# Kernel tuning notes

Measured on AMD Instinct MI355X. Metric: run time of the kernel, lower is better.

The kernel has to match this reference:

```python
import jax, jax.numpy as jnp
import numpy as np

DIM = 1024; H = 16; KVH = 4; HD = 64          # head_dim = DIM // H
I = 2048                                       # intermediate_size = 2*DIM
N = 16                                         # ssm_state_size
DTR = 64                                       # dt_rank = DIM // 16
K = 4                                          # conv kernel
BASE = 10000.0
EPS = 1.1920929e-07                            # torch F.rms_norm default eps (fp32 finfo eps)

def rms_norm(x):
    return x * jax.lax.rsqrt(jnp.mean(x * x, axis=-1, keepdims=True) + EPS)

def rope_tables(S, dims):
    inv = 1.0 / BASE ** (jnp.arange(0, dims, 2, dtype=jnp.float32) / dims)
    f = jnp.outer(jnp.arange(S, dtype=jnp.float32), inv)   # [S, dims//2]
    return jnp.cos(f), jnp.sin(f)

def apply_rope(x, cos, sin):
    half = x.shape[-1] // 2
    x1, x2 = x[..., :half], x[..., half:]
    return jnp.concatenate([x1 * cos + x2 * sin, -x1 * sin + x2 * cos], axis=-1)

def setup_inputs() -> dict:
    key = jax.random.key(0)
    ks = jax.random.split(key, 12)
    B, S = 2, 2048
    def w(k, shape, s=0.02):
        return jax.random.normal(k, shape, jnp.float32) * s
    return {
        "x": jax.random.normal(ks[0], (B, S, DIM), jnp.float32),
        "W_mamba": w(ks[1], (2 * I, DIM)),
        "W_q": w(ks[2], (DIM, DIM)),
        "W_kv": w(ks[3], (2 * KVH * HD, DIM)),
        "q_gain": jnp.full((H,), 1.0, jnp.float32),
        "conv_w": w(ks[4], (I, K), 0.2),
        "conv_b": jnp.zeros((I,), jnp.float32),
        "W_xproj": w(ks[5], (DTR + 2 * N, I)),
        "W_dt": w(ks[6], (I, DTR)),
        "b_dt": w(ks[7], (I,), 0.5),
        "A_log": jnp.log(jnp.broadcast_to(jnp.arange(1, N + 1, dtype=jnp.float32), (I, N))),
        "D": jnp.ones((I,), jnp.float32),
        "W_mamba_out": w(ks[8], (DIM, I)),
        "W_proj": w(ks[9], (DIM, DIM)),
        "merge_alpha": jnp.zeros((1,), jnp.float32),
    }

def reference(x, W_mamba, W_q, W_kv, q_gain, conv_w, conv_b, W_xproj, W_dt, b_dt,
              A_log, D, W_mamba_out, W_proj, merge_alpha):
    B, S, _ = x.shape
    # --- parallel input projection for the mamba branch ---
    mp = x @ W_mamba.T                         # [B,S,2I]
    x_ssm, gate = mp[..., :I], mp[..., I:]
    # --- attention branch (GQA + full RoPE + per-head q gain) ---
    q = (x @ W_q.T).reshape(B, S, H, HD).transpose(0, 2, 1, 3)
    kv = x @ W_kv.T
    k = kv[..., :KVH * HD].reshape(B, S, KVH, HD).transpose(0, 2, 1, 3)
    v = kv[..., KVH * HD:].reshape(B, S, KVH, HD).transpose(0, 2, 1, 3)
    q = rms_norm(q); k = rms_norm(k)
    cos, sin = rope_tables(S, HD)
    q = apply_rope(q, cos, sin)
    k = apply_rope(k, cos, sin)
    q = q * q_gain[None, :, None, None]
    nrep = H // KVH
    k = jnp.repeat(k, nrep, axis=1)
    v = jnp.repeat(v, nrep, axis=1)
    scores = jnp.einsum('bhqd,bhkd->bhqk', q, k) / jnp.sqrt(jnp.float32(HD))
    mask = jnp.tril(jnp.ones((S, S), bool))
    scores = jnp.where(mask, scores, -jnp.inf)
    y = jnp.einsum('bhqk,bhkd->bhqd', jax.nn.softmax(scores, axis=-1), v)
    attn_out = y.transpose(0, 2, 1, 3).reshape(B, S, DIM)
    # --- mamba/SSM branch: causal depthwise conv1d + silu ---
    xc = x_ssm.transpose(0, 2, 1)              # [B,I,S]
    u = jax.lax.conv_general_dilated(xc, conv_w[:, None, :], (1,), [(K - 1, 0)],
                                     dimension_numbers=('NCH', 'OIH', 'NCH'),
                                     feature_group_count=I) + conv_b[None, :, None]
    u = u * jax.nn.sigmoid(u)                  # silu, [B,I,S]
    u_bsi = u.transpose(0, 2, 1)               # [B,S,I]
    params = u_bsi @ W_xproj.T                 # [B,S,DTR+2N]
    dt_low = params[..., :DTR]
    Bm = params[..., DTR:DTR + N]
    Cm = params[..., DTR + N:]
    delta = jax.nn.softplus(dt_low @ W_dt.T + b_dt)   # [B,S,I] (delta_bias + softplus)
    A = -jnp.exp(A_log)                        # [I,N]
    def step(state, inp):
        d_t, b_t, c_t, u_t = inp               # [B,I],[B,N],[B,N],[B,I]
        dA = jnp.exp(d_t[:, :, None] * A[None])
        state = state * dA + d_t[:, :, None] * b_t[:, None, :] * u_t[:, :, None]
        y_t = jnp.sum(state * c_t[:, None, :], axis=-1)
        return state, y_t
    xs = (delta.transpose(1, 0, 2), Bm.transpose(1, 0, 2),
          Cm.transpose(1, 0, 2), u_bsi.transpose(1, 0, 2))
    state0 = jnp.zeros((B, I, N), x.dtype)
    _, ys = jax.lax.scan(step, state0, xs)     # ys: [S,B,I]
    y_ssm = ys.transpose(1, 0, 2) + u_bsi * D  # + D skip
    y_ssm = y_ssm * (gate * jax.nn.sigmoid(gate))      # gated by silu(z)
    mamba_out = y_ssm @ W_mamba_out.T          # [B,S,DIM]
    # --- gated merge + output projection ---
    alpha = jax.nn.sigmoid(merge_alpha)
    merged = alpha * attn_out + (1.0 - alpha) * mamba_out
    return merged @ W_proj.T
```

## Files before the change

kernel.cpp:

```cpp
#include <hip/hip_runtime.h>
#include <hip/hip_bf16.h>

#define B_   2
#define S_   2048
#define T_   4096
#define DIM_ 1024
#define H_   16
#define KVH_ 4
#define HD_  64
#define I_   2048
#define N_   16
#define DTR_ 64
#define MB   ((size_t)1 << 20)

typedef __hip_bfloat16 bf16;
typedef __attribute__((ext_vector_type(8))) short short8;
typedef __attribute__((ext_vector_type(4))) short short4v;
typedef __attribute__((ext_vector_type(4))) float f32x4;

__device__ __forceinline__ float b2f(bf16 v){ return __bfloat162float(v); }
__device__ __forceinline__ bf16  f2b(float v){ return __float2bfloat16(v); }
__device__ __forceinline__ float s2f(short s){
  return __builtin_bit_cast(float, ((unsigned int)(unsigned short)s) << 16);
}
__device__ __forceinline__ short f2s(float v){
  return (short)__builtin_bit_cast(unsigned short, f2b(v));
}

__device__ __forceinline__ void async16(const void* g, void* l) {
  __builtin_amdgcn_global_load_lds((__attribute__((address_space(1))) void*)g,
                                   (__attribute__((address_space(3))) void*)l, 16, 0, 0);
}

__global__ __launch_bounds__(256)
void cast_f2b(const float* __restrict__ in, bf16* __restrict__ out, int n4)
{
  const int i = blockIdx.x * 256 + threadIdx.x;
  if (i >= n4) return;
  const float4 v = ((const float4*)in)[i];
  short4v o;
  o.x = f2s(v.x); o.y = f2s(v.y); o.z = f2s(v.z); o.w = f2s(v.w);
  *(short4v*)(out + (size_t)i * 4) = o;
}

template<int MODE, int TS>
__global__ __launch_bounds__(256)
void gemm_nt(const bf16* __restrict__ A, int lda,
             const bf16* __restrict__ W, int ldw,
             void* __restrict__ C, int ldc,
             bf16* __restrict__ Ct, int ldt,
             const float* __restrict__ bias,
             int M, int N, int K)
{
  __shared__ __align__(16) bf16 As[128*32];
  __shared__ __align__(16) bf16 Bs[128*32];
  const int tid  = threadIdx.x;
  const int lane = tid & 63;
  const int wave = tid >> 6;
  const int l16  = lane & 15;
  const int quad = lane >> 4;
  const int wm   = (wave >> 1) << 6;
  const int wn   = (wave & 1) << 6;
  const int m0   = blockIdx.x << 7;
  const int n0   = blockIdx.y << 7;

  f32x4 acc[4][4];
  const f32x4 zero = {0.f, 0.f, 0.f, 0.f};
  #pragma unroll
  for (int i = 0; i < 4; i++)
    #pragma unroll
    for (int j = 0; j < 4; j++) acc[i][j] = zero;

  for (int k0 = 0; k0 < K; k0 += 32) {
    #pragma unroll
    for (int p = 0; p < 2; p++) {
      const int linear = ((p << 8) + tid) << 4;
      const int row    = linear >> 6;
      const int inrow  = linear & 63;
      async16(A + (size_t)(m0 + row) * lda + k0 + (inrow >> 1), (char*)As + linear);
      int wr = n0 + row; if (wr > N - 1) wr = N - 1;
      async16(W + (size_t)wr * ldw + k0 + (inrow >> 1), (char*)Bs + linear);
    }
    __syncthreads();
    short8 af[4], bfr[4];
    #pragma unroll
    for (int mt = 0; mt < 4; mt++)
      af[mt] = *(const short8*)((const char*)As + ((wm + (mt << 4) + l16) << 6) + (quad << 4));
    #pragma unroll
    for (int nt = 0; nt < 4; nt++)
      bfr[nt] = *(const short8*)((const char*)Bs + ((wn + (nt << 4) + l16) << 6) + (quad << 4));
    #pragma unroll
    for (int mt = 0; mt < 4; mt++)
      #pragma unroll
      for (int nt = 0; nt < 4; nt++)
        acc[mt][nt] = __builtin_amdgcn_mfma_f32_16x16x32_bf16(af[mt], bfr[nt], acc[mt][nt], 0, 0, 0);
    __syncthreads();
  }

  #pragma unroll
  for (int mt = 0; mt < 4; mt++) {
    #pragma unroll
    for (int nt = 0; nt < 4; nt++) {
      const int col = n0 + wn + (nt << 4) + l16;
      if (col >= N) continue;
      const int rowbase = m0 + wm + (mt << 4) + (quad << 2);
      float v[4];
      #pragma unroll
      for (int r = 0; r < 4; r++) {
        float t = acc[mt][nt][r];
        if (MODE == 2) {
          t += bias[col];
          t = (t > 20.f) ? t : log1pf(__expf(t));
        }
        v[r] = t;
      }
      if (TS == 0 || TS == 2) {
        #pragma unroll
        for (int r = 0; r < 4; r++) {
          if (MODE == 0) ((float*)C)[(size_t)(rowbase + r) * ldc + col] = v[r];
          else           ((bf16*)C)[(size_t)(rowbase + r) * ldc + col] = f2b(v[r]);
        }
      }
      if (TS >= 1) {
        short4v p;
        #pragma unroll
        for (int r = 0; r < 4; r++) p[r] = f2s(v[r]);
        *(short4v*)(Ct + (size_t)col * ldt + rowbase) = p;
      }
    }
  }
}

__global__ __launch_bounds__(256)
void qkv_prep(const bf16* __restrict__ qraw, const bf16* __restrict__ kvraw,
              const float* __restrict__ q_gain,
              bf16* __restrict__ qn, bf16* __restrict__ kn, bf16* __restrict__ vt)
{
  const int wid  = blockIdx.x * 4 + (threadIdx.x >> 6);
  const int lane = threadIdx.x & 63;
  const int t    = wid / 24;
  const int slot = wid % 24;
  const int b = t >> 11, s = t & 2047;

  float val;
  if (slot < 16)       val = b2f(qraw [(size_t)t * 1024 + slot * 64 + lane]);
  else if (slot < 20)  val = b2f(kvraw[(size_t)t * 512  + (slot - 16) * 64 + lane]);
  else                 val = b2f(kvraw[(size_t)t * 512  + 256 + (slot - 20) * 64 + lane]);

  if (slot < 20) {
    float ss = val * val;
    #pragma unroll
    for (int off = 32; off; off >>= 1) ss += __shfl_xor(ss, off);
    val *= rsqrtf(ss * (1.0f / 64.0f) + 1.1920929e-07f);
    const int j = lane & 31;
    const float x1 = __shfl(val, j);
    const float x2 = __shfl(val, j + 32);
    const float inv = powf(10000.0f, -(float)j * (1.0f / 32.0f));
    const float ang = (float)s * inv;
    const float c = cosf(ang), sn = sinf(ang);
    val = (lane < 32) ? (x1 * c + x2 * sn) : (x2 * c - x1 * sn);
  }
  if (slot < 16) {
    val *= q_gain[slot];
    qn[((size_t)(b * 16 + slot) * 2048 + s) * 64 + lane] = f2b(val);
  } else if (slot < 20) {
    kn[((size_t)(b * 4 + (slot - 16)) * 2048 + s) * 64 + lane] = f2b(val);
  } else {
    vt[((size_t)(b * 4 + (slot - 20)) * 64 + lane) * 2048 + s] = f2b(val);
  }
}

__global__ __launch_bounds__(256)
void attn_fwd(const bf16* __restrict__ qn, const bf16* __restrict__ kn,
              const bf16* __restrict__ vt, bf16* __restrict__ attn)
{
  __shared__ __align__(16) bf16 Plds[4][16][32];
  const int b = blockIdx.z, h = blockIdx.y, q0 = blockIdx.x * 64;
  const int wave = threadIdx.x >> 6, lane = threadIdx.x & 63;
  const int l16 = lane & 15, quad = lane >> 4;
  const int kvh = h >> 2;
  const bf16* Q  = qn + (size_t)(b * 16 + h)   * 2048 * 64;
  const bf16* Kp = kn + (size_t)(b * 4 + kvh)  * 2048 * 64;
  const bf16* Vt = vt + (size_t)(b * 4 + kvh)  * 64 * 2048;

  const int qrow_l = q0 + wave * 16 + l16;
  const short8 qf0 = *(const short8*)(Q + (size_t)qrow_l * 64 + quad * 8);
  const short8 qf1 = *(const short8*)(Q + (size_t)qrow_l * 64 + 32 + quad * 8);

  f32x4 acc[4];
  const f32x4 zero = {0.f, 0.f, 0.f, 0.f};
  #pragma unroll
  for (int i = 0; i < 4; i++) acc[i] = zero;
  float m_r[4], l_r[4];
  #pragma unroll
  for (int r = 0; r < 4; r++) { m_r[r] = -1e30f; l_r[r] = 0.f; }

  const int nkt = (q0 + 64) >> 5;
  for (int kt = 0; kt < nkt; kt++) {
    const int kb = kt << 5;
    const short8 kfA0 = *(const short8*)(Kp + (size_t)(kb + l16) * 64 + quad * 8);
    const short8 kfA1 = *(const short8*)(Kp + (size_t)(kb + l16) * 64 + 32 + quad * 8);
    const short8 kfB0 = *(const short8*)(Kp + (size_t)(kb + 16 + l16) * 64 + quad * 8);
    const short8 kfB1 = *(const short8*)(Kp + (size_t)(kb + 16 + l16) * 64 + 32 + quad * 8);
    f32x4 sA = zero, sB = zero;
    sA = __builtin_amdgcn_mfma_f32_16x16x32_bf16(qf0, kfA0, sA, 0, 0, 0);
    sA = __builtin_amdgcn_mfma_f32_16x16x32_bf16(qf1, kfA1, sA, 0, 0, 0);
    sB = __builtin_amdgcn_mfma_f32_16x16x32_bf16(qf0, kfB0, sB, 0, 0, 0);
    sB = __builtin_amdgcn_mfma_f32_16x16x32_bf16(qf1, kfB1, sB, 0, 0, 0);

    const int colA = kb + l16, colB = kb + 16 + l16;
    float pA[4], pB[4], alpha[4];
    #pragma unroll
    for (int r = 0; r < 4; r++) {
      const int row = q0 + wave * 16 + quad * 4 + r;
      float a  = sA[r] * 0.125f;
      float bb = sB[r] * 0.125f;
      if (colA > row) a  = -1e30f;
      if (colB > row) bb = -1e30f;
      float tm = fmaxf(a, bb);
      #pragma unroll
      for (int off = 8; off; off >>= 1) tm = fmaxf(tm, __shfl_xor(tm, off));
      const float nm = fmaxf(m_r[r], tm);
      alpha[r] = __expf(m_r[r] - nm);
      m_r[r] = nm;
      const float pa = __expf(a - nm), pb = __expf(bb - nm);
      pA[r] = pa; pB[r] = pb;
      float ps = pa + pb;
      #pragma unroll
      for (int off = 8; off; off >>= 1) ps += __shfl_xor(ps, off);
      l_r[r] = l_r[r] * alpha[r] + ps;
    }
    #pragma unroll
    for (int nt = 0; nt < 4; nt++)
      #pragma unroll
      for (int r = 0; r < 4; r++) acc[nt][r] *= alpha[r];

    __syncthreads();
    #pragma unroll
    for (int r = 0; r < 4; r++) {
      Plds[wave][quad * 4 + r][l16]      = f2b(pA[r]);
      Plds[wave][quad * 4 + r][16 + l16] = f2b(pB[r]);
    }
    __syncthreads();
    const short8 pf = *(const short8*)(&Plds[wave][l16][quad * 8]);
    #pragma unroll
    for (int nt = 0; nt < 4; nt++) {
      const short8 vf = *(const short8*)(Vt + (size_t)(nt * 16 + l16) * 2048 + kb + quad * 8);
      acc[nt] = __builtin_amdgcn_mfma_f32_16x16x32_bf16(pf, vf, acc[nt], 0, 0, 0);
    }
  }

  #pragma unroll
  for (int nt = 0; nt < 4; nt++)
    #pragma unroll
    for (int r = 0; r < 4; r++) {
      const int row = q0 + wave * 16 + quad * 4 + r;
      attn[((size_t)b * 2048 + row) * 1024 + h * 64 + nt * 16 + l16] = f2b(acc[nt][r] / l_r[r]);
    }
}

__global__ __launch_bounds__(256)
void conv_silu_t(const bf16* __restrict__ xssmT, const float* __restrict__ cw,
                 const float* __restrict__ cb,
                 bf16* __restrict__ u, bf16* __restrict__ uT)
{
  const int i = blockIdx.x;
  const int t = blockIdx.y * 256 + threadIdx.x;
  const int s = t & 2047;
  float acc = cb[i];
  #pragma unroll
  for (int kk = 0; kk < 4; kk++) {
    if (s - 3 + kk >= 0)
      acc += s2f(__builtin_bit_cast(short, xssmT[(size_t)i * 4096 + t - 3 + kk])) * cw[i * 4 + kk];
  }
  const float sig = 1.f / (1.f + __expf(-acc));
  const bf16 r = f2b(acc * sig);
  u [(size_t)t * 2048 + i] = r;
  uT[(size_t)i * 4096 + t] = r;
}

__global__ __launch_bounds__(256)
void transpose_bf16(const bf16* __restrict__ in, bf16* __restrict__ out,
                    int R, int C)
{
  __shared__ bf16 tile[64][65];
  const int c0 = blockIdx.x * 64, r0 = blockIdx.y * 64;
  #pragma unroll
  for (int it = 0; it < 2; it++) {
    const int linear = (it * 256 + threadIdx.x) * 8;
    const int r = linear >> 6, cc = linear & 63;
    const short8 v = *(const short8*)(in + (size_t)(r0 + r) * C + c0 + cc);
    #pragma unroll
    for (int k = 0; k < 8; k++)
      tile[r][cc + k] = __builtin_bit_cast(bf16, (unsigned short)v[k]);
  }
  __syncthreads();
  #pragma unroll
  for (int it = 0; it < 2; it++) {
    const int linear = (it * 256 + threadIdx.x) * 8;
    const int oc = linear >> 6, k = linear & 63;
    short8 v;
    #pragma unroll
    for (int kk = 0; kk < 8; kk++)
      v[kk] = (short)__builtin_bit_cast(unsigned short, tile[k + kk][oc]);
    *(short8*)(out + (size_t)(c0 + oc) * R + r0 + k) = v;
  }
}

__global__ __launch_bounds__(256)
void ssm_scan(const bf16* __restrict__ dltT, const bf16* __restrict__ uT,
              const bf16* __restrict__ prmT, const float* __restrict__ A_log,
              const float* __restrict__ Dv, const bf16* __restrict__ gateT,
              bf16* __restrict__ youtT)
{
  __shared__ float Pl[16][17], Fl[16][17], Il[16][17];
  const int blk = blockIdx.x;
  const int b = blk >> 11, i = blk & 2047;
  const int n = threadIdx.x & 15, c = threadIdx.x >> 4;
  const float a  = -__expf(A_log[i * 16 + n]);
  const float Di = Dv[i];
  const size_t rowoff = (size_t)b * 2048 + c * 128;
  const bf16* dp = dltT  + (size_t)i * 4096 + rowoff;
  const bf16* up = uT    + (size_t)i * 4096 + rowoff;
  const bf16* Bp = prmT  + (size_t)(64 + n) * 4096 + rowoff;
  const bf16* Cp = prmT  + (size_t)(80 + n) * 4096 + rowoff;
  const bf16* gp = gateT + (size_t)i * 4096 + rowoff;
  bf16*       yp = youtT + (size_t)i * 4096 + rowoff;

  float P = 1.f, F = 0.f;
  for (int j0 = 0; j0 < 128; j0 += 8) {
    const short8 d8 = *(const short8*)(dp + j0);
    const short8 u8 = *(const short8*)(up + j0);
    const short8 B8 = *(const short8*)(Bp + j0);
    #pragma unroll
    for (int j = 0; j < 8; j++) {
      const float dt = s2f(d8[j]);
      const float dA = __expf(dt * a);
      P *= dA;
      F = F * dA + dt * s2f(u8[j]) * s2f(B8[j]);
    }
  }
  Pl[n][c] = P; Fl[n][c] = F;
  __syncthreads();

  if (threadIdx.x < 16) {
    const int nn = threadIdx.x;
    float s = 0.f;
    #pragma unroll
    for (int cc = 0; cc < 16; cc++) {
      Il[nn][cc] = s;
      s = Fl[nn][cc] + Pl[nn][cc] * s;
    }
  }
  __syncthreads();

  float state = Il[n][c];
  for (int j0 = 0; j0 < 128; j0 += 8) {
    const short8 d8 = *(const short8*)(dp + j0);
    const short8 u8 = *(const short8*)(up + j0);
    const short8 B8 = *(const short8*)(Bp + j0);
    const short8 C8 = *(const short8*)(Cp + j0);
    const short8 g8 = *(const short8*)(gp + j0);
    short8 o8;
    #pragma unroll
    for (int j = 0; j < 8; j++) {
      const float dt = s2f(d8[j]);
      const float ut = s2f(u8[j]);
      const float dA = __expf(dt * a);
      state = state * dA + dt * ut * s2f(B8[j]);
      float y = state * s2f(C8[j]);
      y += __shfl_xor(y, 1); y += __shfl_xor(y, 2);
      y += __shfl_xor(y, 4); y += __shfl_xor(y, 8);
      const float g  = s2f(g8[j]);
      const float gs = g / (1.f + __expf(-g));
      o8[j] = f2s((y + ut * Di) * gs);
    }
    if (n == 0) *(short8*)(yp + j0) = o8;
  }
}

__global__ __launch_bounds__(256)
void merge_k(const bf16* __restrict__ attn, const bf16* __restrict__ mamba,
             const float* __restrict__ malpha, bf16* __restrict__ merged)
{
  const size_t idx = (size_t)blockIdx.x * 256 + threadIdx.x;
  const float al = 1.f / (1.f + __expf(-malpha[0]));
  merged[idx] = f2b(al * b2f(attn[idx]) + (1.f - al) * b2f(mamba[idx]));
}

extern "C" void kernel_launch(void* const* d_in, const int* in_sizes, int n_in,
                              void* d_out, int out_size, void* d_ws, size_t ws_size,
                              hipStream_t stream)
{
  const float* x_f     = (const float*)d_in[0];
  const float* Wm_f    = (const float*)d_in[1];
  const float* Wq_f    = (const float*)d_in[2];
  const float* Wkv_f   = (const float*)d_in[3];
  const float* q_gain  = (const float*)d_in[4];
  const float* conv_w  = (const float*)d_in[5];
  const float* conv_b  = (const float*)d_in[6];
  const float* Wxp_f   = (const float*)d_in[7];
  const float* Wdt_f   = (const float*)d_in[8];
  const float* b_dt    = (const float*)d_in[9];
  const float* A_log   = (const float*)d_in[10];
  const float* Dv      = (const float*)d_in[11];
  const float* Wmo_f   = (const float*)d_in[12];
  const float* Wp_f    = (const float*)d_in[13];
  const float* malpha  = (const float*)d_in[14];

  char* wp = (char*)d_ws;
  bf16*  xb    = (bf16*)(wp + 0 * MB);
  bf16*  Wm_b  = (bf16*)(wp + 8 * MB);
  bf16*  Wq_b  = (bf16*)(wp + 16 * MB);
  bf16*  Wkv_b = (bf16*)(wp + 18 * MB);
  bf16*  xssmT = (bf16*)(wp + 19 * MB);
  bf16*  gateT = (bf16*)(wp + 35 * MB);
  bf16*  u     = (bf16*)(wp + 51 * MB);
  bf16*  uT    = (bf16*)(wp + 67 * MB);
  bf16*  qraw  = (bf16*)(wp + 83 * MB);
  bf16*  kvraw = (bf16*)(wp + 91 * MB);
  bf16*  dltT  = (bf16*)(wp + 95 * MB);
  bf16*  qn    = (bf16*)(wp + 0 * MB);
  bf16*  kn    = (bf16*)(wp + 8 * MB);
  bf16*  vtb   = (bf16*)(wp + 10 * MB);
  bf16*  Wxp_b = (bf16*)(wp + 12 * MB);
  bf16*  Wdt_b = (bf16*)(wp + 12 * MB + 512 * 1024);
  bf16*  prm   = (bf16*)(wp + 13 * MB);
  bf16*  prmT  = (bf16*)(wp + 13 * MB + 768 * 1024);
  bf16*  Wp_b  = (bf16*)(wp + 16 * MB);
  bf16*  attnb = (bf16*)(wp + 83 * MB);
  bf16*  Wmo_b = (bf16*)(wp + 91 * MB);
  bf16*  ybuf  = (bf16*)(wp + 19 * MB);
  bf16*  ybufT = (bf16*)(wp + 51 * MB);
  bf16*  mam   = (bf16*)(wp + 35 * MB);
  bf16*  mrg   = (bf16*)(wp + 43 * MB);
  (void)ws_size; (void)in_sizes; (void)n_in; (void)out_size;

  auto cast = [&](const float* src, bf16* dst, int n) {
    const int n4 = n >> 2;
    cast_f2b<<<dim3((n4 + 255) / 256), 256, 0, stream>>>(src, dst, n4);
  };
  cast(x_f,   xb,    T_ * 1024);
  cast(Wm_f,  Wm_b,  4096 * 1024);
  cast(Wq_f,  Wq_b,  1024 * 1024);
  cast(Wkv_f, Wkv_b, 512 * 1024);

  gemm_nt<1,1><<<dim3(32, 16), 256, 0, stream>>>(xb, 1024, Wm_b,               1024, nullptr, 0, xssmT, 4096, nullptr, T_, 2048, 1024);
  gemm_nt<1,1><<<dim3(32, 16), 256, 0, stream>>>(xb, 1024, Wm_b + 2048 * 1024, 1024, nullptr, 0, gateT, 4096, nullptr, T_, 2048, 1024);
  gemm_nt<1,0><<<dim3(32, 8),  256, 0, stream>>>(xb, 1024, Wq_b,  1024, qraw,  1024, nullptr, 0, nullptr, T_, 1024, 1024);
  gemm_nt<1,0><<<dim3(32, 4),  256, 0, stream>>>(xb, 1024, Wkv_b, 1024, kvraw,  512, nullptr, 0, nullptr, T_,  512, 1024);

  qkv_prep<<<dim3((T_ * 24) / 4), 256, 0, stream>>>(qraw, kvraw, q_gain, qn, kn, vtb);
  conv_silu_t<<<dim3(2048, 16), 256, 0, stream>>>(xssmT, conv_w, conv_b, u, uT);
  attn_fwd<<<dim3(32, 16, 2), 256, 0, stream>>>(qn, kn, vtb, attnb);

  cast(Wxp_f, Wxp_b, 96 * 2048);
  cast(Wdt_f, Wdt_b, 2048 * 64);
  cast(Wmo_f, Wmo_b, 1024 * 2048);
  cast(Wp_f,  Wp_b,  1024 * 1024);

  gemm_nt<1,2><<<dim3(32, 1),  256, 0, stream>>>(u, 2048, Wxp_b, 2048, prm, 96, prmT, 4096, nullptr, T_, 96, 2048);
  gemm_nt<2,1><<<dim3(32, 16), 256, 0, stream>>>(prm, 96, Wdt_b, 64, nullptr, 0, dltT, 4096, b_dt, T_, 2048, 64);
  ssm_scan<<<dim3(4096), 256, 0, stream>>>(dltT, uT, prmT, A_log, Dv, gateT, ybufT);
  transpose_bf16<<<dim3(64, 32), 256, 0, stream>>>(ybufT, ybuf, 2048, 4096);
  gemm_nt<1,0><<<dim3(32, 8),  256, 0, stream>>>(ybuf, 2048, Wmo_b, 2048, mam, 1024, nullptr, 0, nullptr, T_, 1024, 2048);

  merge_k<<<dim3(16384), 256, 0, stream>>>(attnb, mam, malpha, mrg);
  gemm_nt<0,0><<<dim3(32, 8),  256, 0, stream>>>(mrg, 1024, Wp_b, 1024, (float*)d_out, 1024, nullptr, 0, nullptr, T_, 1024, 1024);
}
```

Baseline: 925.6 us.

## Replace strided conv output write with tiled transpose; move gating into transpose kernel

conv_silu_t no longer writes the row-major u buffer with a column-strided, uncoalesced store. u is now produced by a separate tiled LDS transpose of uT. The SiLU gate multiply leaves the scan kernel and joins the final y transpose in a new finish_y kernel, so the scan no longer loads gate or computes sigmoid per step. The cost is one extra kernel launch plus an extra read and write of u, and the scan output is rounded to bf16 before gating.

```diff
diff --git a/kernel.cpp b/kernel.cpp
--- a/kernel.cpp
+++ b/kernel.cpp
@@ -261,8 +261,7 @@
 
 __global__ __launch_bounds__(256)
 void conv_silu_t(const bf16* __restrict__ xssmT, const float* __restrict__ cw,
-                 const float* __restrict__ cb,
-                 bf16* __restrict__ u, bf16* __restrict__ uT)
+                 const float* __restrict__ cb, bf16* __restrict__ uT)
 {
   const int i = blockIdx.x;
   const int t = blockIdx.y * 256 + threadIdx.x;
@@ -274,9 +273,7 @@
       acc += s2f(__builtin_bit_cast(short, xssmT[(size_t)i * 4096 + t - 3 + kk])) * cw[i * 4 + kk];
   }
   const float sig = 1.f / (1.f + __expf(-acc));
-  const bf16 r = f2b(acc * sig);
-  u [(size_t)t * 2048 + i] = r;
-  uT[(size_t)i * 4096 + t] = r;
+  uT[(size_t)i * 4096 + t] = f2b(acc * sig);
 }
 
 __global__ __launch_bounds__(256)
@@ -308,10 +305,42 @@
 }
 
 __global__ __launch_bounds__(256)
+void finish_y(const bf16* __restrict__ yT, const bf16* __restrict__ gT,
+              bf16* __restrict__ out)
+{
+  __shared__ bf16 tile[64][65];
+  const int t0 = blockIdx.x * 64, i0 = blockIdx.y * 64;
+  #pragma unroll
+  for (int it = 0; it < 2; it++) {
+    const int linear = (it * 256 + threadIdx.x) * 8;
+    const int r = linear >> 6, cc = linear & 63;
+    const size_t off = (size_t)(i0 + r) * 4096 + t0 + cc;
+    const short8 y8 = *(const short8*)(yT + off);
+    const short8 g8 = *(const short8*)(gT + off);
+    #pragma unroll
+    for (int k = 0; k < 8; k++) {
+      const float g  = s2f(g8[k]);
+      const float gs = g / (1.f + __expf(-g));
+      tile[r][cc + k] = f2b(s2f(y8[k]) * gs);
+    }
+  }
+  __syncthreads();
+  #pragma unroll
+  for (int it = 0; it < 2; it++) {
+    const int linear = (it * 256 + threadIdx.x) * 8;
+    const int oc = linear >> 6, k = linear & 63;
+    short8 v;
+    #pragma unroll
+    for (int kk = 0; kk < 8; kk++)
+      v[kk] = (short)__builtin_bit_cast(unsigned short, tile[k + kk][oc]);
+    *(short8*)(out + (size_t)(t0 + oc) * 2048 + i0 + k) = v;
+  }
+}
+
+__global__ __launch_bounds__(256)
 void ssm_scan(const bf16* __restrict__ dltT, const bf16* __restrict__ uT,
               const bf16* __restrict__ prmT, const float* __restrict__ A_log,
-              const float* __restrict__ Dv, const bf16* __restrict__ gateT,
-              bf16* __restrict__ youtT)
+              const float* __restrict__ Dv, bf16* __restrict__ youtT)
 {
   __shared__ float Pl[16][17], Fl[16][17], Il[16][17];
   const int blk = blockIdx.x;
@@ -324,7 +353,6 @@
   const bf16* up = uT    + (size_t)i * 4096 + rowoff;
   const bf16* Bp = prmT  + (size_t)(64 + n) * 4096 + rowoff;
   const bf16* Cp = prmT  + (size_t)(80 + n) * 4096 + rowoff;
-  const bf16* gp = gateT + (size_t)i * 4096 + rowoff;
   bf16*       yp = youtT + (size_t)i * 4096 + rowoff;
 
   float P = 1.f, F = 0.f;
@@ -360,7 +388,6 @@
     const short8 u8 = *(const short8*)(up + j0);
     const short8 B8 = *(const short8*)(Bp + j0);
     const short8 C8 = *(const short8*)(Cp + j0);
-    const short8 g8 = *(const short8*)(gp + j0);
     short8 o8;
     #pragma unroll
     for (int j = 0; j < 8; j++) {
@@ -371,9 +398,7 @@
       float y = state * s2f(C8[j]);
       y += __shfl_xor(y, 1); y += __shfl_xor(y, 2);
       y += __shfl_xor(y, 4); y += __shfl_xor(y, 8);
-      const float g  = s2f(g8[j]);
-      const float gs = g / (1.f + __expf(-g));
-      o8[j] = f2s((y + ut * Di) * gs);
+      o8[j] = f2s(y + ut * Di);
     }
     if (n == 0) *(short8*)(yp + j0) = o8;
   }
@@ -451,8 +476,9 @@
   gemm_nt<1,0><<<dim3(32, 4),  256, 0, stream>>>(xb, 1024, Wkv_b, 1024, kvraw,  512, nullptr, 0, nullptr, T_,  512, 1024);
 
   qkv_prep<<<dim3((T_ * 24) / 4), 256, 0, stream>>>(qraw, kvraw, q_gain, qn, kn, vtb);
-  conv_silu_t<<<dim3(2048, 16), 256, 0, stream>>>(xssmT, conv_w, conv_b, u, uT);
+  conv_silu_t<<<dim3(2048, 16), 256, 0, stream>>>(xssmT, conv_w, conv_b, uT);
   attn_fwd<<<dim3(32, 16, 2), 256, 0, stream>>>(qn, kn, vtb, attnb);
+  transpose_bf16<<<dim3(64, 32), 256, 0, stream>>>(uT, u, 2048, 4096);
 
   cast(Wxp_f, Wxp_b, 96 * 2048);
   cast(Wdt_f, Wdt_b, 2048 * 64);
@@ -461,8 +487,8 @@
 
   gemm_nt<1,2><<<dim3(32, 1),  256, 0, stream>>>(u, 2048, Wxp_b, 2048, prm, 96, prmT, 4096, nullptr, T_, 96, 2048);
   gemm_nt<2,1><<<dim3(32, 16), 256, 0, stream>>>(prm, 96, Wdt_b, 64, nullptr, 0, dltT, 4096, b_dt, T_, 2048, 64);
-  ssm_scan<<<dim3(4096), 256, 0, stream>>>(dltT, uT, prmT, A_log, Dv, gateT, ybufT);
-  transpose_bf16<<<dim3(64, 32), 256, 0, stream>>>(ybufT, ybuf, 2048, 4096);
+  ssm_scan<<<dim3(4096), 256, 0, stream>>>(dltT, uT, prmT, A_log, Dv, ybufT);
+  finish_y<<<dim3(64, 32), 256, 0, stream>>>(ybufT, gateT, ybuf);
   gemm_nt<1,0><<<dim3(32, 8),  256, 0, stream>>>(ybuf, 2048, Wmo_b, 2048, mam, 1024, nullptr, 0, nullptr, T_, 1024, 2048);
 
   merge_k<<<dim3(16384), 256, 0, stream>>>(attnb, mam, malpha, mrg);
```

After: 903.9 us. -2.3%, faster.
